# Kernel tuning notes

Measured on AMD Instinct MI355X. Metric: run time of the kernel, lower is better.

## Reference

```python
import jax, jax.numpy as jnp
import numpy as np


def setup_inputs() -> dict:
    key = jax.random.key(0)
    N, T, P = 256, 1024, 4
    kZ, kW, kPhi, kA = jax.random.split(key, 4)
    return {
        "Z": jax.random.uniform(kZ, (N, N, T), dtype=jnp.float32),
        "W": jax.random.uniform(kW, (N, N, T), dtype=jnp.float32),
        "Phi": jax.random.normal(kPhi, (P, N, N), dtype=jnp.float32) * 0.1,
        "alpha": jax.random.normal(kA, (N, T + P), dtype=jnp.float32),
        "num_players": N,
        "num_timesteps": T,
        "AR_order_p": P,
    }


def _log_btl(Z, W, alpha, num_players):
    # Faithful port of compute_log_BTL_vectorized
    T = Z.shape[-1]
    i_idx, j_idx = np.triu_indices(num_players, k=1)  # static edge list
    Z_pairs = Z[i_idx, j_idx, :]          # [n_pairs, T]
    W_pairs = W[i_idx, j_idx, :]          # [n_pairs, T]
    sliced_alpha = alpha[:, -T:]          # [N, T]
    s_i = sliced_alpha[i_idx, :]          # [n_pairs, T]
    s_j = sliced_alpha[j_idx, :]          # [n_pairs, T]
    return (Z_pairs * s_i + W_pairs * s_j
            - (Z_pairs + W_pairs) * jnp.log(jnp.exp(s_i) + jnp.exp(s_j))).sum()


def _ar_error(Phi, alpha, num_timesteps, p):
    # Vectorized over the original per-timestep bmm loop:
    # for t in [p, T): summed_t = sum_k Phi[k] @ alpha[:, t-p+k]
    Tp = num_timesteps - p
    # lags[k, :, t'] = alpha[:, t' + k], t' = t - p
    lags = jnp.stack([alpha[:, k:k + Tp] for k in range(p)], axis=0)  # [p, N, Tp]
    summed = jnp.einsum('knm,kmt->nt', Phi, lags)   # [N, Tp]
    actual = alpha[:, p:num_timesteps]              # [N, Tp]
    # Faithful to torch broadcasting: ([N,1] - [N]) -> [N,N] per timestep
    diff = summed[:, None, :] - actual[None, :, :]  # [N, N, Tp]
    return (diff ** 2).sum()


def reference(Z, W, Phi, alpha, num_players, num_timesteps, AR_order_p):
    log_btl = _log_btl(Z, W, alpha, num_players)
    ar_err = _ar_error(Phi, alpha, num_timesteps, AR_order_p)
    return jnp.stack([log_btl, ar_err])  # [2]
```

## Files before the change

kernel.cpp:

```cpp
#include <hip/hip_runtime.h>
#include <math.h>

#define N_P 256
#define T_T 1024
#define P_AR 4
#define TP (T_T - P_AR)
#define ALPHA_LD (T_T + P_AR)
#define NPAIRS (N_P * (N_P - 1) / 2)
#define MCHUNK 8

__device__ __forceinline__ float block_reduce_sum(float v, float* tmp) {
#pragma unroll
    for (int o = 32; o > 0; o >>= 1) v += __shfl_down(v, o, 64);
    int lane = threadIdx.x & 63;
    int w    = threadIdx.x >> 6;
    if (lane == 0) tmp[w] = v;
    __syncthreads();
    if (threadIdx.x == 0) v = tmp[0] + tmp[1] + tmp[2] + tmp[3];
    return v;
}

__global__ __launch_bounds__(256) void colsum_kernel(const float* __restrict__ alpha,
                                                     float* __restrict__ colsum,
                                                     float* __restrict__ out) {
    __shared__ float tmp[4];
    int t = blockIdx.x * 256 + threadIdx.x;
    float cs = 0.f, sq = 0.f;
    if (t < TP) {
        for (int j = 0; j < N_P; ++j) {
            float a = alpha[j * ALPHA_LD + P_AR + t];
            cs += a;
            sq += a * a;
        }
        colsum[t] = cs;
    }
    float tot = block_reduce_sum(sq, tmp);
    if (threadIdx.x == 0) atomicAdd(out + 1, (float)N_P * tot);
}

__global__ __launch_bounds__(256) void ar_kernel(const float* __restrict__ Phi,
                                                 const float* __restrict__ alpha,
                                                 const float* __restrict__ colsum,
                                                 float* __restrict__ out) {
    __shared__ float phi_s[4 * N_P];
    __shared__ __align__(16) float a_s[MCHUNK * 1024];
    __shared__ float tmp[4];

    const int n   = blockIdx.x;
    const int tid = threadIdx.x;

    for (int x = tid; x < 4 * N_P; x += 256)
        phi_s[x] = Phi[(x >> 8) * (N_P * N_P) + n * N_P + (x & 255)];

    float acc0 = 0.f, acc1 = 0.f, acc2 = 0.f, acc3 = 0.f;
    const int t0 = tid * 4;

    for (int mc = 0; mc < N_P; mc += MCHUNK) {
        __syncthreads();
        for (int x = tid; x < MCHUNK * 256; x += 256) {
            int r = x >> 8, c = x & 255;
            ((float4*)a_s)[r * 256 + c] =
                *(const float4*)(alpha + (size_t)(mc + r) * ALPHA_LD + c * 4);
        }
        __syncthreads();
        if (t0 < TP) {
#pragma unroll
            for (int r = 0; r < MCHUNK; ++r) {
                const float4 av0 = ((const float4*)(a_s + r * 1024))[tid];
                const float4 av1 = ((const float4*)(a_s + r * 1024))[tid + 1];
                int m = mc + r;
                float p0 = phi_s[m];
                float p1 = phi_s[256 + m];
                float p2 = phi_s[512 + m];
                float p3 = phi_s[768 + m];
                acc0 += p0 * av0.x + p1 * av0.y + p2 * av0.z + p3 * av0.w;
                acc1 += p0 * av0.y + p1 * av0.z + p2 * av0.w + p3 * av1.x;
                acc2 += p0 * av0.z + p1 * av0.w + p2 * av1.x + p3 * av1.y;
                acc3 += p0 * av0.w + p1 * av1.x + p2 * av1.y + p3 * av1.z;
            }
        }
    }

    float local = 0.f;
    if (t0 < TP) {
        float c0 = colsum[t0], c1 = colsum[t0 + 1], c2 = colsum[t0 + 2], c3 = colsum[t0 + 3];
        local = 256.f * (acc0 * acc0 + acc1 * acc1 + acc2 * acc2 + acc3 * acc3)
              - 2.f * (acc0 * c0 + acc1 * c1 + acc2 * c2 + acc3 * c3);
    }
    __syncthreads();
    float tot = block_reduce_sum(local, tmp);
    if (tid == 0) atomicAdd(out + 1, tot);
}

__device__ __forceinline__ float btl_term(float z, float w, float a, float b) {
    float m   = fmaxf(a, b);
    float lse = m + __logf(1.f + __expf(-fabsf(a - b)));
    return z * (a - lse) + w * (b - lse);
}

__global__ __launch_bounds__(256) void btl_kernel(const float* __restrict__ Z,
                                                  const float* __restrict__ W,
                                                  const float* __restrict__ alpha,
                                                  float* __restrict__ out) {
    __shared__ float tmp[4];
    const int tid = threadIdx.x;
    float acc = 0.f;

    for (int q = blockIdx.x; q < NPAIRS; q += gridDim.x) {
        int i = (int)((511.0 - sqrt((double)(261121 - 8 * q))) * 0.5);
        if (i < 0) i = 0;
        if (i > 254) i = 254;
        while (i < 254 && ((i + 1) * (511 - (i + 1))) / 2 <= q) ++i;
        while ((i * (511 - i)) / 2 > q) --i;
        int j = q - (i * (511 - i)) / 2 + i + 1;

        const size_t base = (size_t)(i * N_P + j) * T_T + tid * 4;
        const float4 z  = *(const float4*)(Z + base);
        const float4 w  = *(const float4*)(W + base);
        const float4 si = *(const float4*)(alpha + (size_t)i * ALPHA_LD + P_AR + tid * 4);
        const float4 sj = *(const float4*)(alpha + (size_t)j * ALPHA_LD + P_AR + tid * 4);

        acc += btl_term(z.x, w.x, si.x, sj.x);
        acc += btl_term(z.y, w.y, si.y, sj.y);
        acc += btl_term(z.z, w.z, si.z, sj.z);
        acc += btl_term(z.w, w.w, si.w, sj.w);
    }

    float tot = block_reduce_sum(acc, tmp);
    if (tid == 0) atomicAdd(out, tot);
}

extern "C" void kernel_launch(void* const* d_in, const int* in_sizes, int n_in,
                              void* d_out, int out_size, void* d_ws, size_t ws_size,
                              hipStream_t stream) {
    const float* Z     = (const float*)d_in[0];
    const float* W     = (const float*)d_in[1];
    const float* Phi   = (const float*)d_in[2];
    const float* alpha = (const float*)d_in[3];
    float* out    = (float*)d_out;
    float* colsum = (float*)d_ws;

    hipMemsetAsync(d_out, 0, 2 * sizeof(float), stream);
    hipLaunchKernelGGL(colsum_kernel, dim3(4),    dim3(256), 0, stream, alpha, colsum, out);
    hipLaunchKernelGGL(ar_kernel,     dim3(N_P),  dim3(256), 0, stream, Phi, alpha, colsum, out);
    hipLaunchKernelGGL(btl_kernel,    dim3(2040), dim3(256), 0, stream, Z, W, alpha, out);
}
```

Before: 559.0 us.

## Fuse colsum, AR and BTL kernels into one launch with role-split blocks

Merges the three kernels into a single launch. The first 256 blocks do the AR error and the remaining blocks do the BTL sum. Column sums and sum of squares are now computed inside the AR loop from data already in shared memory, which removes the separate colsum kernel and its workspace round trip. The goal is to cut launch overhead and let the small AR work run alongside the bandwidth-bound BTL reduction. The cost is that AR blocks carry a larger shared-memory footprint, which may limit occupancy for BTL blocks, and they add a little extra arithmetic.

```diff
diff --git a/kernel.cpp b/kernel.cpp
--- a/kernel.cpp
+++ b/kernel.cpp
@@ -8,6 +8,8 @@
 #define ALPHA_LD (T_T + P_AR)
 #define NPAIRS (N_P * (N_P - 1) / 2)
 #define MCHUNK 8
+#define AR_BLOCKS 256
+#define BTL_BLOCKS 2040
 
 __device__ __forceinline__ float block_reduce_sum(float v, float* tmp) {
 #pragma unroll
@@ -20,114 +22,95 @@
     return v;
 }
 
-__global__ __launch_bounds__(256) void colsum_kernel(const float* __restrict__ alpha,
-                                                     float* __restrict__ colsum,
-                                                     float* __restrict__ out) {
-    __shared__ float tmp[4];
-    int t = blockIdx.x * 256 + threadIdx.x;
-    float cs = 0.f, sq = 0.f;
-    if (t < TP) {
-        for (int j = 0; j < N_P; ++j) {
-            float a = alpha[j * ALPHA_LD + P_AR + t];
-            cs += a;
-            sq += a * a;
-        }
-        colsum[t] = cs;
-    }
-    float tot = block_reduce_sum(sq, tmp);
-    if (threadIdx.x == 0) atomicAdd(out + 1, (float)N_P * tot);
-}
-
-__global__ __launch_bounds__(256) void ar_kernel(const float* __restrict__ Phi,
-                                                 const float* __restrict__ alpha,
-                                                 const float* __restrict__ colsum,
-                                                 float* __restrict__ out) {
-    __shared__ float phi_s[4 * N_P];
-    __shared__ __align__(16) float a_s[MCHUNK * 1024];
-    __shared__ float tmp[4];
-
-    const int n   = blockIdx.x;
-    const int tid = threadIdx.x;
-
-    for (int x = tid; x < 4 * N_P; x += 256)
-        phi_s[x] = Phi[(x >> 8) * (N_P * N_P) + n * N_P + (x & 255)];
-
-    float acc0 = 0.f, acc1 = 0.f, acc2 = 0.f, acc3 = 0.f;
-    const int t0 = tid * 4;
-
-    for (int mc = 0; mc < N_P; mc += MCHUNK) {
-        __syncthreads();
-        for (int x = tid; x < MCHUNK * 256; x += 256) {
-            int r = x >> 8, c = x & 255;
-            ((float4*)a_s)[r * 256 + c] =
-                *(const float4*)(alpha + (size_t)(mc + r) * ALPHA_LD + c * 4);
-        }
-        __syncthreads();
-        if (t0 < TP) {
-#pragma unroll
-            for (int r = 0; r < MCHUNK; ++r) {
-                const float4 av0 = ((const float4*)(a_s + r * 1024))[tid];
-                const float4 av1 = ((const float4*)(a_s + r * 1024))[tid + 1];
-                int m = mc + r;
-                float p0 = phi_s[m];
-                float p1 = phi_s[256 + m];
-                float p2 = phi_s[512 + m];
-                float p3 = phi_s[768 + m];
-                acc0 += p0 * av0.x + p1 * av0.y + p2 * av0.z + p3 * av0.w;
-                acc1 += p0 * av0.y + p1 * av0.z + p2 * av0.w + p3 * av1.x;
-                acc2 += p0 * av0.z + p1 * av0.w + p2 * av1.x + p3 * av1.y;
-                acc3 += p0 * av0.w + p1 * av1.x + p2 * av1.y + p3 * av1.z;
-            }
-        }
-    }
-
-    float local = 0.f;
-    if (t0 < TP) {
-        float c0 = colsum[t0], c1 = colsum[t0 + 1], c2 = colsum[t0 + 2], c3 = colsum[t0 + 3];
-        local = 256.f * (acc0 * acc0 + acc1 * acc1 + acc2 * acc2 + acc3 * acc3)
-              - 2.f * (acc0 * c0 + acc1 * c1 + acc2 * c2 + acc3 * c3);
-    }
-    __syncthreads();
-    float tot = block_reduce_sum(local, tmp);
-    if (tid == 0) atomicAdd(out + 1, tot);
-}
-
 __device__ __forceinline__ float btl_term(float z, float w, float a, float b) {
     float m   = fmaxf(a, b);
     float lse = m + __logf(1.f + __expf(-fabsf(a - b)));
     return z * (a - lse) + w * (b - lse);
 }
 
-__global__ __launch_bounds__(256) void btl_kernel(const float* __restrict__ Z,
-                                                  const float* __restrict__ W,
-                                                  const float* __restrict__ alpha,
-                                                  float* __restrict__ out) {
+__global__ __launch_bounds__(256) void fused_kernel(const float* __restrict__ Z,
+                                                    const float* __restrict__ W,
+                                                    const float* __restrict__ Phi,
+                                                    const float* __restrict__ alpha,
+                                                    float* __restrict__ out) {
+    __shared__ float phi_s[4 * N_P];
+    __shared__ __align__(16) float a_s[MCHUNK * 1024];
     __shared__ float tmp[4];
+
     const int tid = threadIdx.x;
-    float acc = 0.f;
 
-    for (int q = blockIdx.x; q < NPAIRS; q += gridDim.x) {
-        int i = (int)((511.0 - sqrt((double)(261121 - 8 * q))) * 0.5);
-        if (i < 0) i = 0;
-        if (i > 254) i = 254;
-        while (i < 254 && ((i + 1) * (511 - (i + 1))) / 2 <= q) ++i;
-        while ((i * (511 - i)) / 2 > q) --i;
-        int j = q - (i * (511 - i)) / 2 + i + 1;
+    if (blockIdx.x < AR_BLOCKS) {
+        const int n = blockIdx.x;
 
-        const size_t base = (size_t)(i * N_P + j) * T_T + tid * 4;
-        const float4 z  = *(const float4*)(Z + base);
-        const float4 w  = *(const float4*)(W + base);
-        const float4 si = *(const float4*)(alpha + (size_t)i * ALPHA_LD + P_AR + tid * 4);
-        const float4 sj = *(const float4*)(alpha + (size_t)j * ALPHA_LD + P_AR + tid * 4);
+        for (int x = tid; x < 4 * N_P; x += 256)
+            phi_s[x] = Phi[(x >> 8) * (N_P * N_P) + n * N_P + (x & 255)];
 
-        acc += btl_term(z.x, w.x, si.x, sj.x);
-        acc += btl_term(z.y, w.y, si.y, sj.y);
-        acc += btl_term(z.z, w.z, si.z, sj.z);
-        acc += btl_term(z.w, w.w, si.w, sj.w);
+        float acc0 = 0.f, acc1 = 0.f, acc2 = 0.f, acc3 = 0.f;
+        float cs0 = 0.f, cs1 = 0.f, cs2 = 0.f, cs3 = 0.f;
+        float sq  = 0.f;
+        const int t0 = tid * 4;
+
+        for (int mc = 0; mc < N_P; mc += MCHUNK) {
+            __syncthreads();
+            for (int x = tid; x < MCHUNK * 256; x += 256) {
+                int r = x >> 8, c = x & 255;
+                ((float4*)a_s)[r * 256 + c] =
+                    *(const float4*)(alpha + (size_t)(mc + r) * ALPHA_LD + c * 4);
+            }
+            __syncthreads();
+            if (t0 < TP) {
+#pragma unroll
+                for (int r = 0; r < MCHUNK; ++r) {
+                    const float4 av0 = ((const float4*)(a_s + r * 1024))[tid];
+                    const float4 av1 = ((const float4*)(a_s + r * 1024))[tid + 1];
+                    int m = mc + r;
+                    float p0 = phi_s[m];
+                    float p1 = phi_s[256 + m];
+                    float p2 = phi_s[512 + m];
+                    float p3 = phi_s[768 + m];
+                    acc0 += p0 * av0.x + p1 * av0.y + p2 * av0.z + p3 * av0.w;
+                    acc1 += p0 * av0.y + p1 * av0.z + p2 * av0.w + p3 * av1.x;
+                    acc2 += p0 * av0.z + p1 * av0.w + p2 * av1.x + p3 * av1.y;
+                    acc3 += p0 * av0.w + p1 * av1.x + p2 * av1.y + p3 * av1.z;
+                    cs0 += av1.x; cs1 += av1.y; cs2 += av1.z; cs3 += av1.w;
+                    sq  += av1.x * av1.x + av1.y * av1.y + av1.z * av1.z + av1.w * av1.w;
+                }
+            }
+        }
+
+        float local = 0.f;
+        if (t0 < TP) {
+            local = 256.f * (acc0 * acc0 + acc1 * acc1 + acc2 * acc2 + acc3 * acc3)
+                  - 2.f * (acc0 * cs0 + acc1 * cs1 + acc2 * cs2 + acc3 * cs3);
+            if (n == 0) local += 256.f * sq;
+        }
+        __syncthreads();
+        float tot = block_reduce_sum(local, tmp);
+        if (tid == 0) atomicAdd(out + 1, tot);
+    } else {
+        float acc = 0.f;
+        for (int q = blockIdx.x - AR_BLOCKS; q < NPAIRS; q += BTL_BLOCKS) {
+            int i = (int)((511.0 - sqrt((double)(261121 - 8 * q))) * 0.5);
+            if (i < 0) i = 0;
+            if (i > 254) i = 254;
+            while (i < 254 && ((i + 1) * (511 - (i + 1))) / 2 <= q) ++i;
+            while ((i * (511 - i)) / 2 > q) --i;
+            int j = q - (i * (511 - i)) / 2 + i + 1;
+
+            const size_t base = (size_t)(i * N_P + j) * T_T + tid * 4;
+            const float4 z  = *(const float4*)(Z + base);
+            const float4 w  = *(const float4*)(W + base);
+            const float4 si = *(const float4*)(alpha + (size_t)i * ALPHA_LD + P_AR + tid * 4);
+            const float4 sj = *(const float4*)(alpha + (size_t)j * ALPHA_LD + P_AR + tid * 4);
+
+            acc += btl_term(z.x, w.x, si.x, sj.x);
+            acc += btl_term(z.y, w.y, si.y, sj.y);
+            acc += btl_term(z.z, w.z, si.z, sj.z);
+            acc += btl_term(z.w, w.w, si.w, sj.w);
+        }
+        float tot = block_reduce_sum(acc, tmp);
+        if (tid == 0) atomicAdd(out, tot);
     }
-
-    float tot = block_reduce_sum(acc, tmp);
-    if (tid == 0) atomicAdd(out, tot);
 }
 
 extern "C" void kernel_launch(void* const* d_in, const int* in_sizes, int n_in,
@@ -137,11 +120,9 @@
     const float* W     = (const float*)d_in[1];
     const float* Phi   = (const float*)d_in[2];
     const float* alpha = (const float*)d_in[3];
-    float* out    = (float*)d_out;
-    float* colsum = (float*)d_ws;
+    float* out = (float*)d_out;
 
     hipMemsetAsync(d_out, 0, 2 * sizeof(float), stream);
-    hipLaunchKernelGGL(colsum_kernel, dim3(4),    dim3(256), 0, stream, alpha, colsum, out);
-    hipLaunchKernelGGL(ar_kernel,     dim3(N_P),  dim3(256), 0, stream, Phi, alpha, colsum, out);
-    hipLaunchKernelGGL(btl_kernel,    dim3(2040), dim3(256), 0, stream, Z, W, alpha, out);
+    hipLaunchKernelGGL(fused_kernel, dim3(AR_BLOCKS + BTL_BLOCKS), dim3(256), 0, stream,
+                       Z, W, Phi, alpha, out);
 }
```

New measurement: 499.8 us. -10.6%, faster.
